# Optimization experiments

Hardware: AMD Instinct MI355X
Metric: run time of the kernel (lower is better)

The kernel has to match this reference:

```python
import jax, jax.numpy as jnp
import numpy as np

D_MODEL = 1024
N_HEADS = 16
D_K = D_MODEL // N_HEADS
EPS = 1e-5


def setup_inputs() -> dict:
    key = jax.random.key(0)
    ks = jax.random.split(key, 10)
    s = 1.0 / np.sqrt(D_MODEL)
    x = jax.random.normal(ks[0], (4, 2048, D_MODEL), dtype=jnp.float32)
    def lin(k):
        kw, kb = jax.random.split(k)
        W = jax.random.uniform(kw, (D_MODEL, D_MODEL), jnp.float32, -s, s)
        b = jax.random.uniform(kb, (D_MODEL,), jnp.float32, -s, s)
        return W, b
    Wq, bq = lin(ks[1])
    Wk, bk = lin(ks[2])
    Wv, bv = lin(ks[3])
    Wo, bo = lin(ks[4])
    gamma = jnp.ones((D_MODEL,), jnp.float32)
    beta = jnp.zeros((D_MODEL,), jnp.float32)
    return {"x": x, "Wq": Wq, "bq": bq, "Wk": Wk, "bk": bk,
            "Wv": Wv, "bv": bv, "Wo": Wo, "bo": bo,
            "gamma": gamma, "beta": beta}


def reference(x, Wq, bq, Wk, bk, Wv, bv, Wo, bo, gamma, beta):
    b, n, _ = x.shape
    residual = x
    # projections (PyTorch Linear: x @ W.T + b; here W stored as [in,out]-equivalent via transpose-free matmul)
    q = x @ Wq.T + bq
    k = x @ Wk.T + bk
    v = x @ Wv.T + bv
    # b n (h d) -> b h n d
    q = q.reshape(b, n, N_HEADS, D_K).transpose(0, 2, 1, 3)
    k = k.reshape(b, n, N_HEADS, D_K).transpose(0, 2, 1, 3)
    v = v.reshape(b, n, N_HEADS, D_K).transpose(0, 2, 1, 3)
    scores = jnp.einsum('bhnd,bhmd->bhnm', q, k) / jnp.sqrt(jnp.float32(D_K))
    attn = jax.nn.softmax(scores, axis=-1)
    out = jnp.einsum('bhnm,bhmd->bhnd', attn, v)
    out = out.transpose(0, 2, 1, 3).reshape(b, n, D_MODEL)
    out = out @ Wo.T + bo
    h = residual + out
    mu = jnp.mean(h, axis=-1, keepdims=True)
    var = jnp.var(h, axis=-1, keepdims=True)
    out_ln = (h - mu) / jnp.sqrt(var + EPS) * gamma + beta
    return (out_ln, attn)
```

## Files before the change

kernel.cpp:

```cpp
#include <hip/hip_runtime.h>
#include <math.h>

#define D_MODEL 1024
#define N_HEADS 16
#define D_K     64
#define SEQ     2048
#define BATCH   4
#define EPS     1e-5f
#define NT      (SEQ / 64)

typedef __attribute__((ext_vector_type(8))) short bf16x8;
typedef __attribute__((ext_vector_type(4))) float f32x4;

__device__ __forceinline__ unsigned short f2bf(float f) {
    unsigned u = __float_as_uint(f);
    u += 0x7fff + ((u >> 16) & 1);
    return (unsigned short)(u >> 16);
}

#define GLDS16(g, l) __builtin_amdgcn_global_load_lds( \
    (const __attribute__((address_space(1))) void*)(g), \
    (__attribute__((address_space(3))) void*)(l), 16, 0, 0)

__global__ __launch_bounds__(256) void cvt_f32_bf16(
    const float* __restrict__ in, unsigned short* __restrict__ out, int n4)
{
    int i = blockIdx.x * 256 + threadIdx.x;
    if (i >= n4) return;
    float4 f = ((const float4*)in)[i];
    union { ushort4 u; uint2 v; } o;
    o.u.x = f2bf(f.x); o.u.y = f2bf(f.y); o.u.z = f2bf(f.z); o.u.w = f2bf(f.w);
    ((uint2*)out)[i] = o.v;
}

__global__ __launch_bounds__(256) void gemm_qkv(
    const unsigned short* __restrict__ A,
    const unsigned short* __restrict__ Bq, const unsigned short* __restrict__ Bk,
    const unsigned short* __restrict__ Bv,
    const float* __restrict__ biq, const float* __restrict__ bik,
    const float* __restrict__ biv,
    unsigned short* __restrict__ Oq, unsigned short* __restrict__ Ok,
    unsigned short* __restrict__ Ov)
{
    const int which = blockIdx.x >> 3;
    const unsigned short* B = which == 0 ? Bq : (which == 1 ? Bk : Bv);
    const float* bias        = which == 0 ? biq : (which == 1 ? bik : biv);
    unsigned short* O        = which == 0 ? Oq : (which == 1 ? Ok : Ov);
    const float scale        = which == 0 ? 0.125f : 1.0f;

    __shared__ unsigned short As[128 * 32];
    __shared__ unsigned short Bs[128 * 32];
    const int tid = threadIdx.x;
    const int w = tid >> 6, lane = tid & 63;
    const int l15 = lane & 15, lh = lane >> 4;
    const int wm = w >> 1, wn = w & 1;
    const int bm = blockIdx.y * 128, bn = (blockIdx.x & 7) * 128;
    const int K = D_MODEL, N = D_MODEL;

    const int srow = lane >> 2;
    const int skk  = (lane & 3) * 8;

    f32x4 acc[4][4] = {};

    for (int k0 = 0; k0 < K; k0 += 32) {
#pragma unroll
        for (int cc = 0; cc < 2; ++cc) {
            int chunk = w * 2 + cc;
            int row = chunk * 16 + srow;
            GLDS16(A + (size_t)(bm + row) * K + k0 + skk, As + chunk * 512);
            GLDS16(B + (size_t)(bn + row) * K + k0 + skk, Bs + chunk * 512);
        }
        __syncthreads();
        bf16x8 af[4], bfr[4];
#pragma unroll
        for (int mi = 0; mi < 4; ++mi)
            af[mi] = *(const bf16x8*)&As[(wm * 64 + mi * 16 + l15) * 32 + lh * 8];
#pragma unroll
        for (int nj = 0; nj < 4; ++nj)
            bfr[nj] = *(const bf16x8*)&Bs[(wn * 64 + nj * 16 + l15) * 32 + lh * 8];
#pragma unroll
        for (int mi = 0; mi < 4; ++mi)
#pragma unroll
            for (int nj = 0; nj < 4; ++nj)
                acc[mi][nj] = __builtin_amdgcn_mfma_f32_16x16x32_bf16(
                    af[mi], bfr[nj], acc[mi][nj], 0, 0, 0);
        __syncthreads();
    }

#pragma unroll
    for (int mi = 0; mi < 4; ++mi) {
#pragma unroll
        for (int nj = 0; nj < 4; ++nj) {
            int col = bn + wn * 64 + nj * 16 + l15;
            float bv = bias[col];
#pragma unroll
            for (int r = 0; r < 4; ++r) {
                int row = bm + wm * 64 + mi * 16 + lh * 4 + r;
                O[(size_t)row * N + col] = f2bf((acc[mi][nj][r] + bv) * scale);
            }
        }
    }
}

__global__ __launch_bounds__(256) void gemm_out(
    const unsigned short* __restrict__ A, const unsigned short* __restrict__ B,
    const float* __restrict__ bias, const float* __restrict__ res,
    float* __restrict__ C)
{
    __shared__ unsigned short As[128 * 32];
    __shared__ unsigned short Bs[128 * 32];
    const int tid = threadIdx.x;
    const int w = tid >> 6, lane = tid & 63;
    const int l15 = lane & 15, lh = lane >> 4;
    const int wm = w >> 1, wn = w & 1;
    const int bm = blockIdx.y * 128, bn = blockIdx.x * 128;
    const int K = D_MODEL, N = D_MODEL;

    const int srow = lane >> 2;
    const int skk  = (lane & 3) * 8;

    f32x4 acc[4][4] = {};

    for (int k0 = 0; k0 < K; k0 += 32) {
#pragma unroll
        for (int cc = 0; cc < 2; ++cc) {
            int chunk = w * 2 + cc;
            int row = chunk * 16 + srow;
            GLDS16(A + (size_t)(bm + row) * K + k0 + skk, As + chunk * 512);
            GLDS16(B + (size_t)(bn + row) * K + k0 + skk, Bs + chunk * 512);
        }
        __syncthreads();
        bf16x8 af[4], bfr[4];
#pragma unroll
        for (int mi = 0; mi < 4; ++mi)
            af[mi] = *(const bf16x8*)&As[(wm * 64 + mi * 16 + l15) * 32 + lh * 8];
#pragma unroll
        for (int nj = 0; nj < 4; ++nj)
            bfr[nj] = *(const bf16x8*)&Bs[(wn * 64 + nj * 16 + l15) * 32 + lh * 8];
#pragma unroll
        for (int mi = 0; mi < 4; ++mi)
#pragma unroll
            for (int nj = 0; nj < 4; ++nj)
                acc[mi][nj] = __builtin_amdgcn_mfma_f32_16x16x32_bf16(
                    af[mi], bfr[nj], acc[mi][nj], 0, 0, 0);
        __syncthreads();
    }

#pragma unroll
    for (int mi = 0; mi < 4; ++mi) {
#pragma unroll
        for (int nj = 0; nj < 4; ++nj) {
            int col = bn + wn * 64 + nj * 16 + l15;
            float bv = bias[col];
#pragma unroll
            for (int r = 0; r < 4; ++r) {
                int row = bm + wm * 64 + mi * 16 + lh * 4 + r;
                C[(size_t)row * N + col] = acc[mi][nj][r] + bv + res[(size_t)row * N + col];
            }
        }
    }
}

__global__ __launch_bounds__(256) void transpose_v(
    const unsigned short* __restrict__ v, unsigned short* __restrict__ vt)
{
    __shared__ unsigned short T[64][72];
    const int bh = blockIdx.y, b = bh >> 4, h = bh & 15;
    const int s0 = blockIdx.x * 64;
    const int tid = threadIdx.x;
#pragma unroll
    for (int i = 0; i < 2; ++i) {
        int idx = i * 256 + tid;
        int sr = idx >> 3, dc = idx & 7;
        uint4 t = *(const uint4*)(v + ((size_t)b * SEQ + s0 + sr) * D_MODEL + h * 64 + dc * 8);
        *(uint4*)&T[sr][dc * 8] = t;
    }
    __syncthreads();
#pragma unroll
    for (int i = 0; i < 2; ++i) {
        int idx = i * 256 + tid;
        int d = idx >> 3, sc = idx & 7;
        unsigned short tmp[8];
#pragma unroll
        for (int j = 0; j < 8; ++j) tmp[j] = T[sc * 8 + j][d];
        *(uint4*)(vt + ((size_t)bh * 64 + d) * SEQ + s0 + sc * 8) = *(uint4*)tmp;
    }
}

__device__ __forceinline__ void stage_tile64(
    const unsigned short* __restrict__ gbase, size_t grow_stride,
    unsigned short* lds, int w, int lane)
{
#pragma unroll
    for (int i = 0; i < 2; ++i) {
        int row = i * 32 + w * 8 + (lane >> 3);
        int c   = (lane & 7) ^ (row & 7);
        GLDS16(gbase + (size_t)row * grow_stride + c * 8,
               lds + (size_t)(i * 256 + w * 64) * 8);
    }
}

__global__ __launch_bounds__(256) void attn_pass0(
    const unsigned short* __restrict__ qb, const unsigned short* __restrict__ kb,
    float* __restrict__ invl)
{
    __shared__ unsigned short Ks[2][64 * 64];
    const int bh = blockIdx.x, b = bh >> 4, head = bh & 15;
    const int tid = threadIdx.x;
    const int w = tid >> 6, lane = tid & 63, l15 = lane & 15, lh = lane >> 4;
    const int bq = blockIdx.y * 128 + w * 32;
    const size_t rowbase = (size_t)b * SEQ;
    const unsigned short* Kh = kb + rowbase * D_MODEL + head * 64;

    bf16x8 aq[2][2];
#pragma unroll
    for (int qs = 0; qs < 2; ++qs)
#pragma unroll
        for (int kd = 0; kd < 2; ++kd)
            aq[qs][kd] = *(const bf16x8*)(qb + (rowbase + bq + qs * 16 + l15) * D_MODEL
                                          + head * 64 + kd * 32 + lh * 8);

    float rsum[2] = {0.f, 0.f};

    stage_tile64(Kh, D_MODEL, Ks[0], w, lane);
    __syncthreads();

    for (int kt = 0; kt < NT; ++kt) {
        const int cur = kt & 1;
        if (kt + 1 < NT)
            stage_tile64(Kh + (size_t)(kt + 1) * 64 * D_MODEL, D_MODEL, Ks[cur ^ 1], w, lane);

        const char* kbuf = (const char*)Ks[cur];
        f32x4 s[2][4] = {};
#pragma unroll
        for (int fj = 0; fj < 4; ++fj) {
            int key = fj * 16 + l15;
            bf16x8 kf0 = *(const bf16x8*)(kbuf + key * 128 + ((lh ^ (key & 7)) << 4));
            bf16x8 kf1 = *(const bf16x8*)(kbuf + key * 128 + (((4 + lh) ^ (key & 7)) << 4));
#pragma unroll
            for (int qs = 0; qs < 2; ++qs) {
                s[qs][fj] = __builtin_amdgcn_mfma_f32_16x16x32_bf16(kf0, aq[qs][0], s[qs][fj], 0, 0, 0);
                s[qs][fj] = __builtin_amdgcn_mfma_f32_16x16x32_bf16(kf1, aq[qs][1], s[qs][fj], 0, 0, 0);
            }
        }
#pragma unroll
        for (int qs = 0; qs < 2; ++qs)
#pragma unroll
            for (int fj = 0; fj < 4; ++fj)
                rsum[qs] += (__expf(s[qs][fj][0]) + __expf(s[qs][fj][1]))
                          + (__expf(s[qs][fj][2]) + __expf(s[qs][fj][3]));
        __syncthreads();
    }

#pragma unroll
    for (int qs = 0; qs < 2; ++qs) {
        float v = rsum[qs];
        v += __shfl_xor(v, 16, 64);
        v += __shfl_xor(v, 32, 64);
        if (lh == 0)
            invl[(size_t)bh * SEQ + bq + qs * 16 + l15] = 1.0f / v;
    }
}

__global__ __launch_bounds__(256) void attn_pass1(
    const unsigned short* __restrict__ qb, const unsigned short* __restrict__ kb,
    const unsigned short* __restrict__ vt, const float* __restrict__ invl,
    float* __restrict__ attnP, unsigned short* __restrict__ ctx)
{
    __shared__ unsigned short Ks[2][64 * 64];
    __shared__ unsigned short Vs[2][64 * 64];
    __shared__ unsigned short Ps[4][32 * 72];
    const int bh = blockIdx.x, b = bh >> 4, head = bh & 15;
    const int tid = threadIdx.x;
    const int w = tid >> 6, lane = tid & 63, l15 = lane & 15, lh = lane >> 4;
    const int bq = blockIdx.y * 128 + w * 32;
    const size_t rowbase = (size_t)b * SEQ;
    const unsigned short* Kh = kb + rowbase * D_MODEL + head * 64;
    const unsigned short* Vh = vt + (size_t)bh * 64 * SEQ;
    char* myPs = (char*)&Ps[w][0];

    bf16x8 aq[2][2];
    float invr[2];
    float* pdst[2];
#pragma unroll
    for (int qs = 0; qs < 2; ++qs) {
#pragma unroll
        for (int kd = 0; kd < 2; ++kd)
            aq[qs][kd] = *(const bf16x8*)(qb + (rowbase + bq + qs * 16 + l15) * D_MODEL
                                          + head * 64 + kd * 32 + lh * 8);
        invr[qs] = invl[(size_t)bh * SEQ + bq + qs * 16 + l15];
        pdst[qs] = attnP + ((size_t)bh * SEQ + bq + qs * 16 + l15) * SEQ + lh * 4;
    }

    f32x4 acc[2][4] = {};

    stage_tile64(Kh, D_MODEL, Ks[0], w, lane);
    stage_tile64(Vh, SEQ,     Vs[0], w, lane);
    __syncthreads();

    for (int kt = 0; kt < NT; ++kt) {
        const int cur = kt & 1;
        const int bk = kt * 64;
        if (kt + 1 < NT) {
            stage_tile64(Kh + (size_t)(bk + 64) * D_MODEL, D_MODEL, Ks[cur ^ 1], w, lane);
            stage_tile64(Vh + (size_t)(bk + 64),           SEQ,     Vs[cur ^ 1], w, lane);
        }

        const char* kbuf = (const char*)Ks[cur];
        f32x4 s[2][4] = {};
#pragma unroll
        for (int fj = 0; fj < 4; ++fj) {
            int key = fj * 16 + l15;
            bf16x8 kf0 = *(const bf16x8*)(kbuf + key * 128 + ((lh ^ (key & 7)) << 4));
            bf16x8 kf1 = *(const bf16x8*)(kbuf + key * 128 + (((4 + lh) ^ (key & 7)) << 4));
#pragma unroll
            for (int qs = 0; qs < 2; ++qs) {
                s[qs][fj] = __builtin_amdgcn_mfma_f32_16x16x32_bf16(kf0, aq[qs][0], s[qs][fj], 0, 0, 0);
                s[qs][fj] = __builtin_amdgcn_mfma_f32_16x16x32_bf16(kf1, aq[qs][1], s[qs][fj], 0, 0, 0);
            }
        }

#pragma unroll
        for (int qs = 0; qs < 2; ++qs) {
#pragma unroll
            for (int fj = 0; fj < 4; ++fj) {
                float p0 = __expf(s[qs][fj][0]) * invr[qs];
                float p1 = __expf(s[qs][fj][1]) * invr[qs];
                float p2 = __expf(s[qs][fj][2]) * invr[qs];
                float p3 = __expf(s[qs][fj][3]) * invr[qs];
                float4 st = {p0, p1, p2, p3};
                *(float4*)(pdst[qs] + bk + fj * 16) = st;
                uint2 pk;
                pk.x = ((unsigned)f2bf(p1) << 16) | f2bf(p0);
                pk.y = ((unsigned)f2bf(p3) << 16) | f2bf(p2);
                *(uint2*)(myPs + (qs * 16 + l15) * 144 + fj * 32 + lh * 8) = pk;
            }
        }

        const char* vbuf = (const char*)Vs[cur];
        bf16x8 pb[2][2];
#pragma unroll
        for (int qs = 0; qs < 2; ++qs)
#pragma unroll
            for (int ks = 0; ks < 2; ++ks)
                pb[qs][ks] = *(const bf16x8*)(myPs + (qs * 16 + l15) * 144 + ks * 64 + lh * 16);
#pragma unroll
        for (int db = 0; db < 4; ++db) {
            int d = db * 16 + l15;
            bf16x8 va0 = *(const bf16x8*)(vbuf + d * 128 + ((lh ^ (d & 7)) << 4));
            bf16x8 va1 = *(const bf16x8*)(vbuf + d * 128 + (((4 + lh) ^ (d & 7)) << 4));
#pragma unroll
            for (int qs = 0; qs < 2; ++qs) {
                acc[qs][db] = __builtin_amdgcn_mfma_f32_16x16x32_bf16(va0, pb[qs][0], acc[qs][db], 0, 0, 0);
                acc[qs][db] = __builtin_amdgcn_mfma_f32_16x16x32_bf16(va1, pb[qs][1], acc[qs][db], 0, 0, 0);
            }
        }
        __syncthreads();
    }

#pragma unroll
    for (int qs = 0; qs < 2; ++qs)
#pragma unroll
        for (int db = 0; db < 4; ++db) {
            union { ushort4 u; uint2 v; } o;
            o.u.x = f2bf(acc[qs][db][0]); o.u.y = f2bf(acc[qs][db][1]);
            o.u.z = f2bf(acc[qs][db][2]); o.u.w = f2bf(acc[qs][db][3]);
            *(uint2*)&ctx[(rowbase + bq + qs * 16 + l15) * D_MODEL + head * 64 + db * 16 + lh * 4] = o.v;
        }
}

__global__ __launch_bounds__(256) void layernorm_rows(
    const float* __restrict__ h, const float* __restrict__ gamma,
    const float* __restrict__ beta, float* __restrict__ out)
{
    const size_t row = blockIdx.x;
    const float* hr = h + row * D_MODEL;
    const int tid = threadIdx.x;

    float v[4];
    float s = 0.f;
#pragma unroll
    for (int i = 0; i < 4; ++i) { v[i] = hr[tid + i * 256]; s += v[i]; }
    __shared__ float red[256];
    red[tid] = s;
    __syncthreads();
    for (int st = 128; st > 0; st >>= 1) {
        if (tid < st) red[tid] += red[tid + st];
        __syncthreads();
    }
    float mean = red[0] * (1.0f / D_MODEL);
    __syncthreads();

    float vs = 0.f;
#pragma unroll
    for (int i = 0; i < 4; ++i) { float d = v[i] - mean; vs += d * d; }
    red[tid] = vs;
    __syncthreads();
    for (int st = 128; st > 0; st >>= 1) {
        if (tid < st) red[tid] += red[tid + st];
        __syncthreads();
    }
    float inv = rsqrtf(red[0] * (1.0f / D_MODEL) + EPS);

#pragma unroll
    for (int i = 0; i < 4; ++i) {
        int c = tid + i * 256;
        out[row * D_MODEL + c] = (v[i] - mean) * inv * gamma[c] + beta[c];
    }
}

extern "C" void kernel_launch(void* const* d_in, const int* in_sizes, int n_in,
                              void* d_out, int out_size, void* d_ws, size_t ws_size,
                              hipStream_t stream)
{
    const float* x     = (const float*)d_in[0];
    const float* Wq    = (const float*)d_in[1];
    const float* bq_   = (const float*)d_in[2];
    const float* Wk    = (const float*)d_in[3];
    const float* bk_   = (const float*)d_in[4];
    const float* Wv    = (const float*)d_in[5];
    const float* bv_   = (const float*)d_in[6];
    const float* Wo    = (const float*)d_in[7];
    const float* bo_   = (const float*)d_in[8];
    const float* gamma = (const float*)d_in[9];
    const float* beta  = (const float*)d_in[10];

    const size_t NX = (size_t)BATCH * SEQ * D_MODEL;
    const size_t NW = (size_t)D_MODEL * D_MODEL;

    float* out_ln = (float*)d_out;
    float* attnP  = out_ln + NX;

    unsigned short* x_bf   = (unsigned short*)d_ws;
    unsigned short* wq_bf  = x_bf + NX;
    unsigned short* wk_bf  = wq_bf + NW;
    unsigned short* wv_bf  = wk_bf + NW;
    unsigned short* wo_bf  = wv_bf + NW;
    unsigned short* q_bf   = wo_bf + NW;
    unsigned short* k_bf   = q_bf + NX;
    unsigned short* v_bf   = k_bf + NX;
    unsigned short* ctx_bf = v_bf + NX;
    float* invl = (float*)(ctx_bf + NX);
    unsigned short* vt_bf = x_bf;
    float* hbuf = (float*)q_bf;

    const int M = BATCH * SEQ;

    cvt_f32_bf16<<<(int)(NX / 4 / 256), 256, 0, stream>>>(x, x_bf, (int)(NX / 4));
    cvt_f32_bf16<<<(int)(NW / 4 / 256), 256, 0, stream>>>(Wq, wq_bf, (int)(NW / 4));
    cvt_f32_bf16<<<(int)(NW / 4 / 256), 256, 0, stream>>>(Wk, wk_bf, (int)(NW / 4));
    cvt_f32_bf16<<<(int)(NW / 4 / 256), 256, 0, stream>>>(Wv, wv_bf, (int)(NW / 4));
    cvt_f32_bf16<<<(int)(NW / 4 / 256), 256, 0, stream>>>(Wo, wo_bf, (int)(NW / 4));

    gemm_qkv<<<dim3(24, M / 128), 256, 0, stream>>>(
        x_bf, wq_bf, wk_bf, wv_bf, bq_, bk_, bv_, q_bf, k_bf, v_bf);

    transpose_v<<<dim3(SEQ / 64, BATCH * N_HEADS), 256, 0, stream>>>(v_bf, vt_bf);

    attn_pass0<<<dim3(BATCH * N_HEADS, SEQ / 128), 256, 0, stream>>>(q_bf, k_bf, invl);

    attn_pass1<<<dim3(BATCH * N_HEADS, SEQ / 128), 256, 0, stream>>>(
        q_bf, k_bf, vt_bf, invl, attnP, ctx_bf);

    gemm_out<<<dim3(D_MODEL / 128, M / 128), 256, 0, stream>>>(
        ctx_bf, wo_bf, bo_, x, hbuf);

    layernorm_rows<<<M, 256, 0, stream>>>(hbuf, gamma, beta, out_ln);
}
```

Before: 533.6 us.

## Triple-buffer K tiles and use partial vmcnt waits instead of syncthreads

Pass0 now prefetches K two tiles ahead into a three-slot LDS ring. Pass1 keeps double buffering, but both passes replace __syncthreads with explicit s_waitcnt vmcnt counts plus s_barrier, so outstanding loads (and pass1's attention-probability stores) need not fully drain at each iteration. Pass1's fp32 attention-probability writes become nontemporal stores to reduce cache pollution. The hand-written vmcnt counts depend on the exact number of issued memory ops, and a wrong count would cause a race on LDS data.

Result: slower. 584.0 us (+9.4%).

```diff
diff --git a/kernel.cpp b/kernel.cpp
--- a/kernel.cpp
+++ b/kernel.cpp
@@ -204,7 +204,7 @@
     const unsigned short* __restrict__ qb, const unsigned short* __restrict__ kb,
     float* __restrict__ invl)
 {
-    __shared__ unsigned short Ks[2][64 * 64];
+    __shared__ unsigned short Ks[3][64 * 64];
     const int bh = blockIdx.x, b = bh >> 4, head = bh & 15;
     const int tid = threadIdx.x;
     const int w = tid >> 6, lane = tid & 63, l15 = lane & 15, lh = lane >> 4;
@@ -223,14 +223,18 @@
     float rsum[2] = {0.f, 0.f};
 
     stage_tile64(Kh, D_MODEL, Ks[0], w, lane);
-    __syncthreads();
+    stage_tile64(Kh + (size_t)64 * D_MODEL, D_MODEL, Ks[1], w, lane);
+    asm volatile("s_waitcnt vmcnt(0)" ::: "memory");
+    __builtin_amdgcn_s_barrier();
+    __builtin_amdgcn_sched_barrier(0);
 
     for (int kt = 0; kt < NT; ++kt) {
-        const int cur = kt & 1;
-        if (kt + 1 < NT)
-            stage_tile64(Kh + (size_t)(kt + 1) * 64 * D_MODEL, D_MODEL, Ks[cur ^ 1], w, lane);
-
-        const char* kbuf = (const char*)Ks[cur];
+        if (kt + 2 < NT)
+            stage_tile64(Kh + (size_t)(kt + 2) * 64 * D_MODEL, D_MODEL,
+                         Ks[(kt + 2) % 3], w, lane);
+        __builtin_amdgcn_sched_barrier(0);
+
+        const char* kbuf = (const char*)Ks[kt % 3];
         f32x4 s[2][4] = {};
 #pragma unroll
         for (int fj = 0; fj < 4; ++fj) {
@@ -249,7 +253,13 @@
             for (int fj = 0; fj < 4; ++fj)
                 rsum[qs] += (__expf(s[qs][fj][0]) + __expf(s[qs][fj][1]))
                           + (__expf(s[qs][fj][2]) + __expf(s[qs][fj][3]));
-        __syncthreads();
+
+        if (kt + 1 < NT) {
+            if (kt + 2 < NT) { asm volatile("s_waitcnt vmcnt(2)" ::: "memory"); }
+            else             { asm volatile("s_waitcnt vmcnt(0)" ::: "memory"); }
+            __builtin_amdgcn_s_barrier();
+            __builtin_amdgcn_sched_barrier(0);
+        }
     }
 
 #pragma unroll
@@ -296,7 +306,9 @@
 
     stage_tile64(Kh, D_MODEL, Ks[0], w, lane);
     stage_tile64(Vh, SEQ,     Vs[0], w, lane);
-    __syncthreads();
+    asm volatile("s_waitcnt vmcnt(0)" ::: "memory");
+    __builtin_amdgcn_s_barrier();
+    __builtin_amdgcn_sched_barrier(0);
 
     for (int kt = 0; kt < NT; ++kt) {
         const int cur = kt & 1;
@@ -305,6 +317,7 @@
             stage_tile64(Kh + (size_t)(bk + 64) * D_MODEL, D_MODEL, Ks[cur ^ 1], w, lane);
             stage_tile64(Vh + (size_t)(bk + 64),           SEQ,     Vs[cur ^ 1], w, lane);
         }
+        __builtin_amdgcn_sched_barrier(0);
 
         const char* kbuf = (const char*)Ks[cur];
         f32x4 s[2][4] = {};
@@ -328,8 +341,8 @@
                 float p1 = __expf(s[qs][fj][1]) * invr[qs];
                 float p2 = __expf(s[qs][fj][2]) * invr[qs];
                 float p3 = __expf(s[qs][fj][3]) * invr[qs];
-                float4 st = {p0, p1, p2, p3};
-                *(float4*)(pdst[qs] + bk + fj * 16) = st;
+                f32x4 st = {p0, p1, p2, p3};
+                __builtin_nontemporal_store(st, (f32x4*)(pdst[qs] + bk + fj * 16));
                 uint2 pk;
                 pk.x = ((unsigned)f2bf(p1) << 16) | f2bf(p0);
                 pk.y = ((unsigned)f2bf(p3) << 16) | f2bf(p2);
@@ -355,7 +368,12 @@
                 acc[qs][db] = __builtin_amdgcn_mfma_f32_16x16x32_bf16(va1, pb[qs][1], acc[qs][db], 0, 0, 0);
             }
         }
-        __syncthreads();
+
+        if (kt + 1 < NT) {
+            asm volatile("s_waitcnt vmcnt(8)" ::: "memory");
+            __builtin_amdgcn_s_barrier();
+            __builtin_amdgcn_sched_barrier(0);
+        }
     }
 
 #pragma unroll
```
